# Kernel optimization log

Hardware: AMD Instinct MI355X
Metric: run time of the kernel (lower is better)

The kernel has to match this reference:

```python
import jax, jax.numpy as jnp
import numpy as np

B, H, S, D = 2, 16, 2048, 64

def setup_inputs() -> dict:
    key = jax.random.key(0)
    k1, k2, k3 = jax.random.split(key, 3)
    Q = jax.random.normal(k1, (B, H, S, D), dtype=jnp.float32)
    K = jax.random.normal(k2, (B, H, S, D), dtype=jnp.float32)
    V = jax.random.normal(k3, (B, H, S, D), dtype=jnp.float32)
    mask = jnp.zeros((S, S), dtype=bool)  # original default: all-False mask
    return {"Q": Q, "K": K, "V": V, "mask": mask}

def reference(Q, K, V, mask) -> jnp.ndarray:
    # Faithful to the original: dk is the KEY SEQUENCE LENGTH (K.size(-2)),
    # and masked_fill(-1e10) happens BEFORE dividing by sqrt(dk).
    dk = K.shape[-2]
    scores = jnp.einsum('bhqd,bhkd->bhqk', Q, K)          # [B,H,S,S]
    scores = jnp.where(mask, -1e10, scores) / jnp.sqrt(jnp.float32(dk))
    attn = jax.nn.softmax(scores, axis=-1)
    return jnp.einsum('bhqk,bhkd->bhqd', attn, V)
```

## Files before the change

kernel.cpp:

```cpp
#include <hip/hip_runtime.h>

#define SQ   2048
#define DD   64
#define BK   64
#define BQ   128
#define LDW  72
#define NT   32

typedef _Float16 f16x8 __attribute__((ext_vector_type(8)));
typedef _Float16 f16x4 __attribute__((ext_vector_type(4)));
typedef float    f32x4 __attribute__((ext_vector_type(4)));

__global__ __launch_bounds__(256, 2)
void attn_fused3(const float* __restrict__ Qg,
                 const float* __restrict__ Kg,
                 const float* __restrict__ Vg,
                 const unsigned char* __restrict__ maskg,
                 float* __restrict__ Og)
{
    __shared__ _Float16 Kl[2][BK * LDW];
    __shared__ _Float16 Vt[2][DD * LDW];

    const int tid  = threadIdx.x;
    const int lane = tid & 63;
    const int w    = tid >> 6;
    const int quad = lane >> 4;
    const int l16  = lane & 15;

    const int n     = blockIdx.x;
    const int bh    = (n & 7) + 8 * ((n >> 3) & 3);
    const int qtile = n >> 5;
    const int qBase = qtile * BQ;

    const float scale  = 0.02209708691207961f;
    const float MASKED = -1e10f * 0.02209708691207961f;

    f16x8 qf[2][2];
#pragma unroll
    for (int qg = 0; qg < 2; ++qg) {
        const float* qrow = Qg + ((size_t)bh * SQ + qBase + w * 32 + qg * 16 + l16) * DD;
#pragma unroll
        for (int h = 0; h < 2; ++h) {
            float4 a = *(const float4*)(qrow + h * 32 + quad * 8);
            float4 b = *(const float4*)(qrow + h * 32 + quad * 8 + 4);
            qf[qg][h][0] = (_Float16)(a.x * scale); qf[qg][h][1] = (_Float16)(a.y * scale);
            qf[qg][h][2] = (_Float16)(a.z * scale); qf[qg][h][3] = (_Float16)(a.w * scale);
            qf[qg][h][4] = (_Float16)(b.x * scale); qf[qg][h][5] = (_Float16)(b.y * scale);
            qf[qg][h][6] = (_Float16)(b.z * scale); qf[qg][h][7] = (_Float16)(b.w * scale);
        }
    }

    f32x4 acc[2][4];
#pragma unroll
    for (int qg = 0; qg < 2; ++qg)
#pragma unroll
        for (int d = 0; d < 4; ++d) acc[qg][d] = (f32x4){0.f, 0.f, 0.f, 0.f};
    float lsum[2] = {0.f, 0.f};

    const int sr  = tid >> 2;
    const int sc4 = (tid & 3) * 16;
    const int vq  = tid & 15;
    const int vdb = (tid >> 4) * 4;
    const int ctw  = vq >> 2, qdw = vq & 3;
    const int keyp = (ctw >> 1) * 32 + qdw * 8 + (ctw & 1) * 4;

    const float* Kbase = Kg + (size_t)bh * SQ * DD;
    const float* Vbase = Vg + (size_t)bh * SQ * DD;
    const unsigned char* mbase = maskg + (size_t)(qBase + (tid >> 1)) * SQ + (tid & 1) * 32;

    {
        const float* ks = Kbase + (size_t)sr * DD + sc4;
        float4 k0v = *(const float4*)(ks + 0), k1v = *(const float4*)(ks + 4);
        float4 k2v = *(const float4*)(ks + 8), k3v = *(const float4*)(ks + 12);
        float4 v0, v1, v2, v3;
        v0 = *(const float4*)(Vbase + (size_t)(vq * 4 + 0) * DD + vdb);
        v1 = *(const float4*)(Vbase + (size_t)(vq * 4 + 1) * DD + vdb);
        v2 = *(const float4*)(Vbase + (size_t)(vq * 4 + 2) * DD + vdb);
        v3 = *(const float4*)(Vbase + (size_t)(vq * 4 + 3) * DD + vdb);
        f16x8 y0, y1;
        y0[0]=(_Float16)k0v.x; y0[1]=(_Float16)k0v.y; y0[2]=(_Float16)k0v.z; y0[3]=(_Float16)k0v.w;
        y0[4]=(_Float16)k1v.x; y0[5]=(_Float16)k1v.y; y0[6]=(_Float16)k1v.z; y0[7]=(_Float16)k1v.w;
        y1[0]=(_Float16)k2v.x; y1[1]=(_Float16)k2v.y; y1[2]=(_Float16)k2v.z; y1[3]=(_Float16)k2v.w;
        y1[4]=(_Float16)k3v.x; y1[5]=(_Float16)k3v.y; y1[6]=(_Float16)k3v.z; y1[7]=(_Float16)k3v.w;
        *(f16x8*)&Kl[0][sr * LDW + sc4]     = y0;
        *(f16x8*)&Kl[0][sr * LDW + sc4 + 8] = y1;
        f16x4 t0 = {(_Float16)v0.x,(_Float16)v1.x,(_Float16)v2.x,(_Float16)v3.x};
        f16x4 t1 = {(_Float16)v0.y,(_Float16)v1.y,(_Float16)v2.y,(_Float16)v3.y};
        f16x4 t2 = {(_Float16)v0.z,(_Float16)v1.z,(_Float16)v2.z,(_Float16)v3.z};
        f16x4 t3 = {(_Float16)v0.w,(_Float16)v1.w,(_Float16)v2.w,(_Float16)v3.w};
        *(f16x4*)&Vt[0][(vdb + 0) * LDW + keyp] = t0;
        *(f16x4*)&Vt[0][(vdb + 1) * LDW + keyp] = t1;
        *(f16x4*)&Vt[0][(vdb + 2) * LDW + keyp] = t2;
        *(f16x4*)&Vt[0][(vdb + 3) * LDW + keyp] = t3;
    }
    uint4 ma = *(const uint4*)(mbase), mb = *(const uint4*)(mbase + 16);
    int tm = __syncthreads_or((int)(ma.x | ma.y | ma.z | ma.w | mb.x | mb.y | mb.z | mb.w));

#pragma unroll 2
    for (int kt = 0; kt < NT; ++kt) {
        const int cur = kt & 1;
        const bool more = (kt + 1 < NT);

        float4 kx[4], vx[4]; uint4 ma2 = {0,0,0,0}, mb2 = {0,0,0,0};
        if (more) {
            const int k0n = (kt + 1) * BK;
            const float* ks = Kbase + (size_t)(k0n + sr) * DD + sc4;
            kx[0] = *(const float4*)(ks + 0);  kx[1] = *(const float4*)(ks + 4);
            kx[2] = *(const float4*)(ks + 8);  kx[3] = *(const float4*)(ks + 12);
            const float* vb = Vbase + (size_t)(k0n + vq * 4) * DD + vdb;
            vx[0] = *(const float4*)(vb);           vx[1] = *(const float4*)(vb + DD);
            vx[2] = *(const float4*)(vb + 2 * DD);  vx[3] = *(const float4*)(vb + 3 * DD);
            ma2 = *(const uint4*)(mbase + k0n);
            mb2 = *(const uint4*)(mbase + k0n + 16);
        }

        f32x4 sA[4], sB[4];
#pragma unroll
        for (int ct = 0; ct < 4; ++ct) {
            f16x8 kf0 = *(const f16x8*)&Kl[cur][(ct * 16 + l16) * LDW + quad * 8];
            f16x8 kf1 = *(const f16x8*)&Kl[cur][(ct * 16 + l16) * LDW + 32 + quad * 8];
            f32x4 c0 = (f32x4){0.f, 0.f, 0.f, 0.f};
            c0 = __builtin_amdgcn_mfma_f32_16x16x32_f16(kf0, qf[0][0], c0, 0, 0, 0);
            c0 = __builtin_amdgcn_mfma_f32_16x16x32_f16(kf1, qf[0][1], c0, 0, 0, 0);
            sA[ct] = c0;
            f32x4 c1 = (f32x4){0.f, 0.f, 0.f, 0.f};
            c1 = __builtin_amdgcn_mfma_f32_16x16x32_f16(kf0, qf[1][0], c1, 0, 0, 0);
            c1 = __builtin_amdgcn_mfma_f32_16x16x32_f16(kf1, qf[1][1], c1, 0, 0, 0);
            sB[ct] = c1;
        }

        if (tm) {
#pragma unroll
            for (int qg = 0; qg < 2; ++qg) {
                const int qgq = qBase + w * 32 + qg * 16 + l16;
#pragma unroll
                for (int ct = 0; ct < 4; ++ct)
#pragma unroll
                    for (int r = 0; r < 4; ++r) {
                        const int kg = kt * BK + ct * 16 + quad * 4 + r;
                        if (maskg[(size_t)qgq * SQ + kg]) {
                            if (qg == 0) sA[ct][r] = MASKED; else sB[ct][r] = MASKED;
                        }
                    }
            }
        }

        f16x4 pA[4], pB[4];
        float ls0 = 0.f, ls1 = 0.f;
#pragma unroll
        for (int ct = 0; ct < 4; ++ct) {
#pragma unroll
            for (int r = 0; r < 4; ++r) {
                const float ea = __expf(sA[ct][r]);
                const float eb = __expf(sB[ct][r]);
                ls0 += ea; ls1 += eb;
                pA[ct][r] = (_Float16)ea;
                pB[ct][r] = (_Float16)eb;
            }
        }
        lsum[0] += ls0; lsum[1] += ls1;

#pragma unroll
        for (int dt = 0; dt < 4; ++dt) {
#pragma unroll
            for (int cp = 0; cp < 2; ++cp) {
                f16x8 vv = *(const f16x8*)&Vt[cur][(dt * 16 + l16) * LDW + cp * 32 + quad * 8];
                f16x4 vlo = {vv[0], vv[1], vv[2], vv[3]};
                f16x4 vhi = {vv[4], vv[5], vv[6], vv[7]};
                acc[0][dt] = __builtin_amdgcn_mfma_f32_16x16x16f16(pA[cp*2+0], vlo, acc[0][dt], 0, 0, 0);
                acc[0][dt] = __builtin_amdgcn_mfma_f32_16x16x16f16(pA[cp*2+1], vhi, acc[0][dt], 0, 0, 0);
                acc[1][dt] = __builtin_amdgcn_mfma_f32_16x16x16f16(pB[cp*2+0], vlo, acc[1][dt], 0, 0, 0);
                acc[1][dt] = __builtin_amdgcn_mfma_f32_16x16x16f16(pB[cp*2+1], vhi, acc[1][dt], 0, 0, 0);
            }
        }

        if (more) {
            f16x8 y0, y1;
            y0[0]=(_Float16)kx[0].x; y0[1]=(_Float16)kx[0].y; y0[2]=(_Float16)kx[0].z; y0[3]=(_Float16)kx[0].w;
            y0[4]=(_Float16)kx[1].x; y0[5]=(_Float16)kx[1].y; y0[6]=(_Float16)kx[1].z; y0[7]=(_Float16)kx[1].w;
            y1[0]=(_Float16)kx[2].x; y1[1]=(_Float16)kx[2].y; y1[2]=(_Float16)kx[2].z; y1[3]=(_Float16)kx[2].w;
            y1[4]=(_Float16)kx[3].x; y1[5]=(_Float16)kx[3].y; y1[6]=(_Float16)kx[3].z; y1[7]=(_Float16)kx[3].w;
            *(f16x8*)&Kl[cur ^ 1][sr * LDW + sc4]     = y0;
            *(f16x8*)&Kl[cur ^ 1][sr * LDW + sc4 + 8] = y1;
            f16x4 t0 = {(_Float16)vx[0].x,(_Float16)vx[1].x,(_Float16)vx[2].x,(_Float16)vx[3].x};
            f16x4 t1 = {(_Float16)vx[0].y,(_Float16)vx[1].y,(_Float16)vx[2].y,(_Float16)vx[3].y};
            f16x4 t2 = {(_Float16)vx[0].z,(_Float16)vx[1].z,(_Float16)vx[2].z,(_Float16)vx[3].z};
            f16x4 t3 = {(_Float16)vx[0].w,(_Float16)vx[1].w,(_Float16)vx[2].w,(_Float16)vx[3].w};
            *(f16x4*)&Vt[cur ^ 1][(vdb + 0) * LDW + keyp] = t0;
            *(f16x4*)&Vt[cur ^ 1][(vdb + 1) * LDW + keyp] = t1;
            *(f16x4*)&Vt[cur ^ 1][(vdb + 2) * LDW + keyp] = t2;
            *(f16x4*)&Vt[cur ^ 1][(vdb + 3) * LDW + keyp] = t3;
        }
        tm = __syncthreads_or((int)(ma2.x | ma2.y | ma2.z | ma2.w | mb2.x | mb2.y | mb2.z | mb2.w));
    }

#pragma unroll
    for (int qg = 0; qg < 2; ++qg) {
        float l = lsum[qg];
        l += __shfl_xor(l, 16);
        l += __shfl_xor(l, 32);
        float lrow[4];
#pragma unroll
        for (int r = 0; r < 4; ++r) lrow[r] = __shfl(l, quad * 4 + r);
        float* ob = Og + ((size_t)bh * SQ + qBase + w * 32 + qg * 16) * DD;
#pragma unroll
        for (int r = 0; r < 4; ++r) {
            const float inv = 1.0f / lrow[r];
            const int qr = quad * 4 + r;
#pragma unroll
            for (int dt = 0; dt < 4; ++dt)
                ob[qr * DD + dt * 16 + l16] = acc[qg][dt][r] * inv;
        }
    }
}

extern "C" void kernel_launch(void* const* d_in, const int* in_sizes, int n_in,
                              void* d_out, int out_size, void* d_ws, size_t ws_size,
                              hipStream_t stream) {
    const float* Q = (const float*)d_in[0];
    const float* K = (const float*)d_in[1];
    const float* V = (const float*)d_in[2];
    const unsigned char* mask = (const unsigned char*)d_in[3];
    float* Out = (float*)d_out;
    attn_fused3<<<dim3(32 * 16), dim3(256), 0, stream>>>(Q, K, V, mask, Out);
}
```

Before: 161.1 us.

## Split key tile across two warp groups with 512 threads and exp2 softmax

Doubles the block to 512 threads, with two groups of four waves each handling half of every 64-key tile, and adds a shared-memory reduction of partial accumulators and row sums at the end. Global loads are split so half the threads stage K and half stage V. The P·V product now uses the wider 16x16x32 MFMA. Scores are pre-scaled by log2(e) so exp2 can replace exp, and conversions use packed round-toward-zero f16 converts. The goal is more waves per CU and less per-thread work, at the cost of an extra reduction pass, more register and barrier pressure, and slightly different rounding.

```diff
diff --git a/kernel.cpp b/kernel.cpp
--- a/kernel.cpp
+++ b/kernel.cpp
@@ -6,47 +6,66 @@
 #define BQ   128
 #define LDW  72
 #define NT   32
+#define BUFH (BK * LDW)
 
 typedef _Float16 f16x8 __attribute__((ext_vector_type(8)));
 typedef _Float16 f16x4 __attribute__((ext_vector_type(4)));
+typedef _Float16 f16x2 __attribute__((ext_vector_type(2)));
 typedef float    f32x4 __attribute__((ext_vector_type(4)));
 
-__global__ __launch_bounds__(256, 2)
-void attn_fused3(const float* __restrict__ Qg,
+#if __has_builtin(__builtin_amdgcn_exp2f)
+#define EXP2F(x) __builtin_amdgcn_exp2f(x)
+#else
+#define EXP2F(x) exp2f(x)
+#endif
+
+static __device__ __forceinline__ f16x2 PKRTZ(float a, float b) {
+    typedef __fp16 fp16x2_t __attribute__((ext_vector_type(2)));
+    union { fp16x2_t i; f16x2 o; } u;
+    u.i = __builtin_amdgcn_cvt_pkrtz(a, b);
+    return u.o;
+}
+#define MFMA32(a, b, c) __builtin_amdgcn_mfma_f32_16x16x32_f16((a), (b), (c), 0, 0, 0)
+
+__global__ __launch_bounds__(512, 4)
+void attn_fused4(const float* __restrict__ Qg,
                  const float* __restrict__ Kg,
                  const float* __restrict__ Vg,
                  const unsigned char* __restrict__ maskg,
                  float* __restrict__ Og)
 {
-    __shared__ _Float16 Kl[2][BK * LDW];
-    __shared__ _Float16 Vt[2][DD * LDW];
+    __shared__ __align__(16) _Float16 smem[4 * BUFH];
 
     const int tid  = threadIdx.x;
     const int lane = tid & 63;
     const int w    = tid >> 6;
     const int quad = lane >> 4;
     const int l16  = lane & 15;
+    const int qw   = w & 3;
+    const int kh   = w >> 2;
 
     const int n     = blockIdx.x;
     const int bh    = (n & 7) + 8 * ((n >> 3) & 3);
     const int qtile = n >> 5;
     const int qBase = qtile * BQ;
 
-    const float scale  = 0.02209708691207961f;
-    const float MASKED = -1e10f * 0.02209708691207961f;
+    const float QSCALE = 0.02209708691207961f * 1.4426950408889634f;
+    const float MASKED = -1e10f * (0.02209708691207961f * 1.4426950408889634f);
 
     f16x8 qf[2][2];
 #pragma unroll
     for (int qg = 0; qg < 2; ++qg) {
-        const float* qrow = Qg + ((size_t)bh * SQ + qBase + w * 32 + qg * 16 + l16) * DD;
+        const float* qrow = Qg + ((size_t)bh * SQ + qBase + qw * 32 + qg * 16 + l16) * DD;
 #pragma unroll
         for (int h = 0; h < 2; ++h) {
             float4 a = *(const float4*)(qrow + h * 32 + quad * 8);
             float4 b = *(const float4*)(qrow + h * 32 + quad * 8 + 4);
-            qf[qg][h][0] = (_Float16)(a.x * scale); qf[qg][h][1] = (_Float16)(a.y * scale);
-            qf[qg][h][2] = (_Float16)(a.z * scale); qf[qg][h][3] = (_Float16)(a.w * scale);
-            qf[qg][h][4] = (_Float16)(b.x * scale); qf[qg][h][5] = (_Float16)(b.y * scale);
-            qf[qg][h][6] = (_Float16)(b.z * scale); qf[qg][h][7] = (_Float16)(b.w * scale);
+            union { f16x8 v; f16x2 p[4]; } u;
+            u.p[0] = PKRTZ(a.x * QSCALE, a.y * QSCALE);
+            u.p[1] = PKRTZ(a.z * QSCALE, a.w * QSCALE);
+            u.p[2] = PKRTZ(b.x * QSCALE, b.y * QSCALE);
+            u.p[3] = PKRTZ(b.z * QSCALE, b.w * QSCALE);
+            qf[qg][h] = u.v;
         }
     }
 
@@ -57,159 +76,180 @@
         for (int d = 0; d < 4; ++d) acc[qg][d] = (f32x4){0.f, 0.f, 0.f, 0.f};
     float lsum[2] = {0.f, 0.f};
 
-    const int sr  = tid >> 2;
-    const int sc4 = (tid & 3) * 16;
-    const int vq  = tid & 15;
-    const int vdb = (tid >> 4) * 4;
+    const bool isK = tid < 256;
+    const int t2   = tid & 255;
+    const int sr   = t2 >> 2;
+    const int sc4  = (t2 & 3) * 16;
+    const int vq   = t2 & 15;
+    const int vdb  = (t2 >> 4) * 4;
     const int ctw  = vq >> 2, qdw = vq & 3;
     const int keyp = (ctw >> 1) * 32 + qdw * 8 + (ctw & 1) * 4;
 
     const float* Kbase = Kg + (size_t)bh * SQ * DD;
     const float* Vbase = Vg + (size_t)bh * SQ * DD;
-    const unsigned char* mbase = maskg + (size_t)(qBase + (tid >> 1)) * SQ + (tid & 1) * 32;
-
-    {
+    const unsigned char* mbase = maskg
+        + (size_t)(qBase + qw * 32 + (lane >> 1)) * SQ + kh * 32 + (lane & 1) * 16;
+
+    if (isK) {
         const float* ks = Kbase + (size_t)sr * DD + sc4;
-        float4 k0v = *(const float4*)(ks + 0), k1v = *(const float4*)(ks + 4);
-        float4 k2v = *(const float4*)(ks + 8), k3v = *(const float4*)(ks + 12);
-        float4 v0, v1, v2, v3;
-        v0 = *(const float4*)(Vbase + (size_t)(vq * 4 + 0) * DD + vdb);
-        v1 = *(const float4*)(Vbase + (size_t)(vq * 4 + 1) * DD + vdb);
-        v2 = *(const float4*)(Vbase + (size_t)(vq * 4 + 2) * DD + vdb);
-        v3 = *(const float4*)(Vbase + (size_t)(vq * 4 + 3) * DD + vdb);
-        f16x8 y0, y1;
-        y0[0]=(_Float16)k0v.x; y0[1]=(_Float16)k0v.y; y0[2]=(_Float16)k0v.z; y0[3]=(_Float16)k0v.w;
-        y0[4]=(_Float16)k1v.x; y0[5]=(_Float16)k1v.y; y0[6]=(_Float16)k1v.z; y0[7]=(_Float16)k1v.w;
-        y1[0]=(_Float16)k2v.x; y1[1]=(_Float16)k2v.y; y1[2]=(_Float16)k2v.z; y1[3]=(_Float16)k2v.w;
-        y1[4]=(_Float16)k3v.x; y1[5]=(_Float16)k3v.y; y1[6]=(_Float16)k3v.z; y1[7]=(_Float16)k3v.w;
-        *(f16x8*)&Kl[0][sr * LDW + sc4]     = y0;
-        *(f16x8*)&Kl[0][sr * LDW + sc4 + 8] = y1;
-        f16x4 t0 = {(_Float16)v0.x,(_Float16)v1.x,(_Float16)v2.x,(_Float16)v3.x};
-        f16x4 t1 = {(_Float16)v0.y,(_Float16)v1.y,(_Float16)v2.y,(_Float16)v3.y};
-        f16x4 t2 = {(_Float16)v0.z,(_Float16)v1.z,(_Float16)v2.z,(_Float16)v3.z};
-        f16x4 t3 = {(_Float16)v0.w,(_Float16)v1.w,(_Float16)v2.w,(_Float16)v3.w};
-        *(f16x4*)&Vt[0][(vdb + 0) * LDW + keyp] = t0;
-        *(f16x4*)&Vt[0][(vdb + 1) * LDW + keyp] = t1;
-        *(f16x4*)&Vt[0][(vdb + 2) * LDW + keyp] = t2;
-        *(f16x4*)&Vt[0][(vdb + 3) * LDW + keyp] = t3;
-    }
-    uint4 ma = *(const uint4*)(mbase), mb = *(const uint4*)(mbase + 16);
-    int tm = __syncthreads_or((int)(ma.x | ma.y | ma.z | ma.w | mb.x | mb.y | mb.z | mb.w));
+        float4 x0 = *(const float4*)(ks),     x1 = *(const float4*)(ks + 4);
+        float4 x2 = *(const float4*)(ks + 8), x3 = *(const float4*)(ks + 12);
+        union { f16x8 v; f16x2 p[4]; } y0, y1;
+        y0.p[0] = PKRTZ(x0.x, x0.y); y0.p[1] = PKRTZ(x0.z, x0.w);
+        y0.p[2] = PKRTZ(x1.x, x1.y); y0.p[3] = PKRTZ(x1.z, x1.w);
+        y1.p[0] = PKRTZ(x2.x, x2.y); y1.p[1] = PKRTZ(x2.z, x2.w);
+        y1.p[2] = PKRTZ(x3.x, x3.y); y1.p[3] = PKRTZ(x3.z, x3.w);
+        *(f16x8*)&smem[sr * LDW + sc4]     = y0.v;
+        *(f16x8*)&smem[sr * LDW + sc4 + 8] = y1.v;
+    } else {
+        const float* vb = Vbase + (size_t)(vq * 4) * DD + vdb;
+        float4 v0 = *(const float4*)(vb);
+        float4 v1 = *(const float4*)(vb + DD);
+        float4 v2 = *(const float4*)(vb + 2 * DD);
+        float4 v3 = *(const float4*)(vb + 3 * DD);
+        _Float16* VT = smem + 2 * BUFH;
+        union { f16x4 v; f16x2 p[2]; } t;
+        t.p[0] = PKRTZ(v0.x, v1.x); t.p[1] = PKRTZ(v2.x, v3.x);
+        *(f16x4*)&VT[(vdb + 0) * LDW + keyp] = t.v;
+        t.p[0] = PKRTZ(v0.y, v1.y); t.p[1] = PKRTZ(v2.y, v3.y);
+        *(f16x4*)&VT[(vdb + 1) * LDW + keyp] = t.v;
+        t.p[0] = PKRTZ(v0.z, v1.z); t.p[1] = PKRTZ(v2.z, v3.z);
+        *(f16x4*)&VT[(vdb + 2) * LDW + keyp] = t.v;
+        t.p[0] = PKRTZ(v0.w, v1.w); t.p[1] = PKRTZ(v2.w, v3.w);
+        *(f16x4*)&VT[(vdb + 3) * LDW + keyp] = t.v;
+    }
+    uint4 ma = *(const uint4*)mbase;
+    int tm = __any((int)(ma.x | ma.y | ma.z | ma.w));
+    __syncthreads();
 
 #pragma unroll 2
     for (int kt = 0; kt < NT; ++kt) {
         const int cur = kt & 1;
         const bool more = (kt + 1 < NT);
-
-        float4 kx[4], vx[4]; uint4 ma2 = {0,0,0,0}, mb2 = {0,0,0,0};
+        _Float16* Kc = smem + cur * BUFH;
+        _Float16* Vc = smem + 2 * BUFH + cur * BUFH;
+
+        float4 x0, x1, x2, x3;
+        uint4 ma2 = {0u, 0u, 0u, 0u};
         if (more) {
             const int k0n = (kt + 1) * BK;
-            const float* ks = Kbase + (size_t)(k0n + sr) * DD + sc4;
-            kx[0] = *(const float4*)(ks + 0);  kx[1] = *(const float4*)(ks + 4);
-            kx[2] = *(const float4*)(ks + 8);  kx[3] = *(const float4*)(ks + 12);
-            const float* vb = Vbase + (size_t)(k0n + vq * 4) * DD + vdb;
-            vx[0] = *(const float4*)(vb);           vx[1] = *(const float4*)(vb + DD);
-            vx[2] = *(const float4*)(vb + 2 * DD);  vx[3] = *(const float4*)(vb + 3 * DD);
+            if (isK) {
+                const float* ks = Kbase + (size_t)(k0n + sr) * DD + sc4;
+                x0 = *(const float4*)(ks);     x1 = *(const float4*)(ks + 4);
+                x2 = *(const float4*)(ks + 8); x3 = *(const float4*)(ks + 12);
+            } else {
+                const float* vb = Vbase + (size_t)(k0n + vq * 4) * DD + vdb;
+                x0 = *(const float4*)(vb);          x1 = *(const float4*)(vb + DD);
+                x2 = *(const float4*)(vb + 2 * DD); x3 = *(const float4*)(vb + 3 * DD);
+            }
             ma2 = *(const uint4*)(mbase + k0n);
-            mb2 = *(const uint4*)(mbase + k0n + 16);
-        }
-
-        f32x4 sA[4], sB[4];
-#pragma unroll
-        for (int ct = 0; ct < 4; ++ct) {
-            f16x8 kf0 = *(const f16x8*)&Kl[cur][(ct * 16 + l16) * LDW + quad * 8];
-            f16x8 kf1 = *(const f16x8*)&Kl[cur][(ct * 16 + l16) * LDW + 32 + quad * 8];
-            f32x4 c0 = (f32x4){0.f, 0.f, 0.f, 0.f};
-            c0 = __builtin_amdgcn_mfma_f32_16x16x32_f16(kf0, qf[0][0], c0, 0, 0, 0);
-            c0 = __builtin_amdgcn_mfma_f32_16x16x32_f16(kf1, qf[0][1], c0, 0, 0, 0);
-            sA[ct] = c0;
-            f32x4 c1 = (f32x4){0.f, 0.f, 0.f, 0.f};
-            c1 = __builtin_amdgcn_mfma_f32_16x16x32_f16(kf0, qf[1][0], c1, 0, 0, 0);
-            c1 = __builtin_amdgcn_mfma_f32_16x16x32_f16(kf1, qf[1][1], c1, 0, 0, 0);
-            sB[ct] = c1;
+        }
+
+        f32x4 sA[2][2];
+#pragma unroll
+        for (int c = 0; c < 2; ++c) {
+            const int krow = (kh * 2 + c) * 16 + l16;
+            f16x8 kf0 = *(const f16x8*)&Kc[krow * LDW + quad * 8];
+            f16x8 kf1 = *(const f16x8*)&Kc[krow * LDW + 32 + quad * 8];
+#pragma unroll
+            for (int qg = 0; qg < 2; ++qg) {
+                f32x4 cc = (f32x4){0.f, 0.f, 0.f, 0.f};
+                cc = MFMA32(kf0, qf[qg][0], cc);
+                cc = MFMA32(kf1, qf[qg][1], cc);
+                sA[qg][c] = cc;
+            }
         }
 
         if (tm) {
 #pragma unroll
             for (int qg = 0; qg < 2; ++qg) {
-                const int qgq = qBase + w * 32 + qg * 16 + l16;
-#pragma unroll
-                for (int ct = 0; ct < 4; ++ct)
+                const size_t qq = (size_t)(qBase + qw * 32 + qg * 16 + l16) * SQ;
+#pragma unroll
+                for (int c = 0; c < 2; ++c)
 #pragma unroll
                     for (int r = 0; r < 4; ++r) {
-                        const int kg = kt * BK + ct * 16 + quad * 4 + r;
-                        if (maskg[(size_t)qgq * SQ + kg]) {
-                            if (qg == 0) sA[ct][r] = MASKED; else sB[ct][r] = MASKED;
-                        }
+                        const int kg = kt * BK + kh * 32 + c * 16 + quad * 4 + r;
+                        if (maskg[qq + kg]) sA[qg][c][r] = MASKED;
                     }
             }
         }
 
-        f16x4 pA[4], pB[4];
-        float ls0 = 0.f, ls1 = 0.f;
-#pragma unroll
-        for (int ct = 0; ct < 4; ++ct) {
+        union { f16x8 v; f16x2 p[4]; } pf[2];
+#pragma unroll
+        for (int qg = 0; qg < 2; ++qg) {
+            float e0 = EXP2F(sA[qg][0][0]), e1 = EXP2F(sA[qg][0][1]);
+            float e2 = EXP2F(sA[qg][0][2]), e3 = EXP2F(sA[qg][0][3]);
+            float e4 = EXP2F(sA[qg][1][0]), e5 = EXP2F(sA[qg][1][1]);
+            float e6 = EXP2F(sA[qg][1][2]), e7 = EXP2F(sA[qg][1][3]);
+            lsum[qg] += ((e0 + e1) + (e2 + e3)) + ((e4 + e5) + (e6 + e7));
+            pf[qg].p[0] = PKRTZ(e0, e1); pf[qg].p[1] = PKRTZ(e2, e3);
+            pf[qg].p[2] = PKRTZ(e4, e5); pf[qg].p[3] = PKRTZ(e6, e7);
+        }
+
+#pragma unroll
+        for (int dt = 0; dt < 4; ++dt) {
+            f16x8 vv = *(const f16x8*)&Vc[(dt * 16 + l16) * LDW + kh * 32 + quad * 8];
+            acc[0][dt] = MFMA32(pf[0].v, vv, acc[0][dt]);
+            acc[1][dt] = MFMA32(pf[1].v, vv, acc[1][dt]);
+        }
+
+        if (more) {
+            _Float16* Kn = smem + (cur ^ 1) * BUFH;
+            _Float16* Vn = smem + 2 * BUFH + (cur ^ 1) * BUFH;
+            if (isK) {
+                union { f16x8 v; f16x2 p[4]; } y0, y1;
+                y0.p[0] = PKRTZ(x0.x, x0.y); y0.p[1] = PKRTZ(x0.z, x0.w);
+                y0.p[2] = PKRTZ(x1.x, x1.y); y0.p[3] = PKRTZ(x1.z, x1.w);
+                y1.p[0] = PKRTZ(x2.x, x2.y); y1.p[1] = PKRTZ(x2.z, x2.w);
+                y1.p[2] = PKRTZ(x3.x, x3.y); y1.p[3] = PKRTZ(x3.z, x3.w);
+                *(f16x8*)&Kn[sr * LDW + sc4]     = y0.v;
+                *(f16x8*)&Kn[sr * LDW + sc4 + 8] = y1.v;
+            } else {
+                union { f16x4 v; f16x2 p[2]; } t;
+                t.p[0] = PKRTZ(x0.x, x1.x); t.p[1] = PKRTZ(x2.x, x3.x);
+                *(f16x4*)&Vn[(vdb + 0) * LDW + keyp] = t.v;
+                t.p[0] = PKRTZ(x0.y, x1.y); t.p[1] = PKRTZ(x2.y, x3.y);
+                *(f16x4*)&Vn[(vdb + 1) * LDW + keyp] = t.v;
+                t.p[0] = PKRTZ(x0.z, x1.z); t.p[1] = PKRTZ(x2.z, x3.z);
+                *(f16x4*)&Vn[(vdb + 2) * LDW + keyp] = t.v;
+                t.p[0] = PKRTZ(x0.w, x1.w); t.p[1] = PKRTZ(x2.w, x3.w);
+                *(f16x4*)&Vn[(vdb + 3) * LDW + keyp] = t.v;
+            }
+        }
+        tm = __any((int)(ma2.x | ma2.y | ma2.z | ma2.w));
+        __syncthreads();
+    }
+
+    float* M = (float*)smem;
+    const int slot = qw * 2;
+    if (kh) {
+#pragma unroll
+        for (int qg = 0; qg < 2; ++qg) {
+#pragma unroll
+            for (int dt = 0; dt < 4; ++dt)
+                *(f32x4*)&M[(((slot + qg) * 4 + dt) * 64 + lane) * 4] = acc[qg][dt];
+            M[8192 + (slot + qg) * 64 + lane] = lsum[qg];
+        }
+    }
+    __syncthreads();
+    if (!kh) {
+#pragma unroll
+        for (int qg = 0; qg < 2; ++qg) {
+#pragma unroll
+            for (int dt = 0; dt < 4; ++dt)
+                acc[qg][dt] += *(const f32x4*)&M[(((slot + qg) * 4 + dt) * 64 + lane) * 4];
+            float l = lsum[qg] + M[8192 + (slot + qg) * 64 + lane];
+            l += __shfl_xor(l, 16);
+            l += __shfl_xor(l, 32);
+            float* ob = Og + ((size_t)bh * SQ + qBase + qw * 32 + qg * 16) * DD;
 #pragma unroll
             for (int r = 0; r < 4; ++r) {
-                const float ea = __expf(sA[ct][r]);
-                const float eb = __expf(sB[ct][r]);
-                ls0 += ea; ls1 += eb;
-                pA[ct][r] = (_Float16)ea;
-                pB[ct][r] = (_Float16)eb;
-            }
-        }
-        lsum[0] += ls0; lsum[1] += ls1;
-
-#pragma unroll
-        for (int dt = 0; dt < 4; ++dt) {
-#pragma unroll
-            for (int cp = 0; cp < 2; ++cp) {
-                f16x8 vv = *(const f16x8*)&Vt[cur][(dt * 16 + l16) * LDW + cp * 32 + quad * 8];
-                f16x4 vlo = {vv[0], vv[1], vv[2], vv[3]};
-                f16x4 vhi = {vv[4], vv[5], vv[6], vv[7]};
-                acc[0][dt] = __builtin_amdgcn_mfma_f32_16x16x16f16(pA[cp*2+0], vlo, acc[0][dt], 0, 0, 0);
-                acc[0][dt] = __builtin_amdgcn_mfma_f32_16x16x16f16(pA[cp*2+1], vhi, acc[0][dt], 0, 0, 0);
-                acc[1][dt] = __builtin_amdgcn_mfma_f32_16x16x16f16(pB[cp*2+0], vlo, acc[1][dt], 0, 0, 0);
-                acc[1][dt] = __builtin_amdgcn_mfma_f32_16x16x16f16(pB[cp*2+1], vhi, acc[1][dt], 0, 0, 0);
-            }
-        }
-
-        if (more) {
-            f16x8 y0, y1;
-            y0[0]=(_Float16)kx[0].x; y0[1]=(_Float16)kx[0].y; y0[2]=(_Float16)kx[0].z; y0[3]=(_Float16)kx[0].w;
-            y0[4]=(_Float16)kx[1].x; y0[5]=(_Float16)kx[1].y; y0[6]=(_Float16)kx[1].z; y0[7]=(_Float16)kx[1].w;
-            y1[0]=(_Float16)kx[2].x; y1[1]=(_Float16)kx[2].y; y1[2]=(_Float16)kx[2].z; y1[3]=(_Float16)kx[2].w;
-            y1[4]=(_Float16)kx[3].x; y1[5]=(_Float16)kx[3].y; y1[6]=(_Float16)kx[3].z; y1[7]=(_Float16)kx[3].w;
-            *(f16x8*)&Kl[cur ^ 1][sr * LDW + sc4]     = y0;
-            *(f16x8*)&Kl[cur ^ 1][sr * LDW + sc4 + 8] = y1;
-            f16x4 t0 = {(_Float16)vx[0].x,(_Float16)vx[1].x,(_Float16)vx[2].x,(_Float16)vx[3].x};
-            f16x4 t1 = {(_Float16)vx[0].y,(_Float16)vx[1].y,(_Float16)vx[2].y,(_Float16)vx[3].y};
-            f16x4 t2 = {(_Float16)vx[0].z,(_Float16)vx[1].z,(_Float16)vx[2].z,(_Float16)vx[3].z};
-            f16x4 t3 = {(_Float16)vx[0].w,(_Float16)vx[1].w,(_Float16)vx[2].w,(_Float16)vx[3].w};
-            *(f16x4*)&Vt[cur ^ 1][(vdb + 0) * LDW + keyp] = t0;
-            *(f16x4*)&Vt[cur ^ 1][(vdb + 1) * LDW + keyp] = t1;
-            *(f16x4*)&Vt[cur ^ 1][(vdb + 2) * LDW + keyp] = t2;
-            *(f16x4*)&Vt[cur ^ 1][(vdb + 3) * LDW + keyp] = t3;
-        }
-        tm = __syncthreads_or((int)(ma2.x | ma2.y | ma2.z | ma2.w | mb2.x | mb2.y | mb2.z | mb2.w));
-    }
-
-#pragma unroll
-    for (int qg = 0; qg < 2; ++qg) {
-        float l = lsum[qg];
-        l += __shfl_xor(l, 16);
-        l += __shfl_xor(l, 32);
-        float lrow[4];
-#pragma unroll
-        for (int r = 0; r < 4; ++r) lrow[r] = __shfl(l, quad * 4 + r);
-        float* ob = Og + ((size_t)bh * SQ + qBase + w * 32 + qg * 16) * DD;
-#pragma unroll
-        for (int r = 0; r < 4; ++r) {
-            const float inv = 1.0f / lrow[r];
-            const int qr = quad * 4 + r;
-#pragma unroll
-            for (int dt = 0; dt < 4; ++dt)
-                ob[qr * DD + dt * 16 + l16] = acc[qg][dt][r] * inv;
+                const float inv = 1.0f / __shfl(l, quad * 4 + r);
+                const int qr = quad * 4 + r;
+#pragma unroll
+                for (int dt = 0; dt < 4; ++dt)
+                    ob[qr * DD + dt * 16 + l16] = acc[qg][dt][r] * inv;
+            }
         }
     }
 }
@@ -222,5 +262,5 @@
     const float* V = (const float*)d_in[2];
     const unsigned char* mask = (const unsigned char*)d_in[3];
     float* Out = (float*)d_out;
-    attn_fused3<<<dim3(32 * 16), dim3(256), 0, stream>>>(Q, K, V, mask, Out);
+    attn_fused4<<<dim3(32 * 16), dim3(512), 0, stream>>>(Q, K, V, mask, Out);
 }
```

Result: slower. 290.4 us (+80.3%).
